# Optimization experiments

Measured on AMD Instinct MI355X. Metric: run time of the kernel, lower is better.

The kernel has to match this reference:

```python
import jax, jax.numpy as jnp
import numpy as np

B, N, E = 2, 5000, 160000
F_IN, HID, ED = 128, 128, 16
IN_EDGE = 2 * F_IN + 16 + ED  # source, target, radial(4*4), edge_attr


def _lin(k, fan_in, fan_out):
    return (jax.random.normal(k, (fan_in, fan_out), jnp.float32) / np.sqrt(fan_in)).astype(jnp.float32)


def setup_inputs() -> dict:
    key = jax.random.key(0)
    ks = jax.random.split(key, 16)
    h = jax.random.normal(ks[0], (B, N, F_IN), jnp.float32)
    coord = jax.random.normal(ks[1], (B, N, 4, 3), jnp.float32)
    edge_index = jax.random.randint(ks[2], (2, E), 0, N)
    edge_attr = jax.random.normal(ks[3], (E, ED), jnp.float32)
    return {
        "h": h, "coord": coord, "edge_index": edge_index, "edge_attr": edge_attr,
        # edge_mlp: Linear(IN_EDGE->HID), ReLU, Linear(HID->HID), ReLU
        "W_e1": _lin(ks[4], IN_EDGE, HID), "b_e1": jnp.zeros((HID,), jnp.float32),
        "W_e2": _lin(ks[5], HID, HID), "b_e2": jnp.zeros((HID,), jnp.float32),
        # node_mlp: Linear(HID+F_IN->HID), ReLU, Linear(HID->F_IN)
        "W_n1": _lin(ks[6], HID + F_IN, HID), "b_n1": jnp.zeros((HID,), jnp.float32),
        "W_n2": _lin(ks[7], HID, F_IN), "b_n2": jnp.zeros((F_IN,), jnp.float32),
        # coord_mlp: Linear(HID->HID), ReLU, Linear(HID->4, bias=False, xavier gain 0.001)
        "W_c1": _lin(ks[8], HID, HID), "b_c1": jnp.zeros((HID,), jnp.float32),
        "W_c2": _lin(ks[9], HID, 4) * 0.001,
    }


def reference(h, coord, edge_index, edge_attr,
              W_e1, b_e1, W_e2, b_e2,
              W_n1, b_n1, W_n2, b_n2,
              W_c1, b_c1, W_c2):
    row, col = edge_index[0], edge_index[1]
    coords_weight = 1.0
    n_nodes = h.shape[1]

    def single(h_b, coord_b):
        # coord2radial
        cd = coord_b[row] - coord_b[col]                                  # [E,4,3]
        prod = jnp.einsum('ejt,ekt->ejk', cd, cd).reshape(cd.shape[0], -1)  # [E,16]
        nrm = jnp.linalg.norm(prod, axis=-1, keepdims=True)
        radial = prod / jnp.maximum(nrm, 1e-12)                           # F.normalize
        # edge_model
        x = jnp.concatenate([h_b[row], h_b[col], radial, edge_attr], axis=-1)
        ef = jax.nn.relu(jax.nn.relu(x @ W_e1 + b_e1) @ W_e2 + b_e2)      # [E,HID]
        # coord_model: segment mean of cd * coord_mlp(ef)
        w = jax.nn.relu(ef @ W_c1 + b_c1) @ W_c2                          # [E,4]
        trans = cd * w[:, :, None]                                        # [E,4,3]
        agg_c = jax.ops.segment_sum(trans, row, num_segments=n_nodes)     # [N,4,3]
        cnt = jax.ops.segment_sum(jnp.ones((row.shape[0],), trans.dtype), row,
                                  num_segments=n_nodes)                   # [N]
        coord_new = coord_b + (agg_c / jnp.maximum(cnt, 1.0)[:, None, None]) * coords_weight
        # node_model (recurrent)
        agg_h = jax.ops.segment_sum(ef, row, num_segments=n_nodes)        # [N,HID]
        z = jnp.concatenate([h_b, agg_h], axis=-1)
        h_new = h_b + jax.nn.relu(z @ W_n1 + b_n1) @ W_n2 + b_n2
        return h_new, coord_new

    hs, coords = jax.vmap(single)(h, coord)
    return hs, coords
```

## Files before the change

### kernel.cpp

```cpp
#include <hip/hip_runtime.h>
#include <hip/hip_bf16.h>

#define B   2
#define NN_ 5000
#define NE_ 160000
#define F   128
#define HID 128
#define ED  16

typedef __bf16 bf16x8 __attribute__((ext_vector_type(8)));
typedef __bf16 bf16x4 __attribute__((ext_vector_type(4)));
typedef float  f32x4  __attribute__((ext_vector_type(4)));

#define MS  136
#define PS  40
#define EDG 64
#define ZS  264
#define HS  136
#define NPB2 32

__global__ __launch_bounds__(512) void pack_hist_kernel(
    const float* __restrict__ We1, const float* __restrict__ We2,
    const float* __restrict__ Wc1, const float* __restrict__ Wc2,
    const float* __restrict__ Wn1, const float* __restrict__ Wn2,
    const int* __restrict__ ei,
    const float* __restrict__ h, const float* __restrict__ be1,
    __bf16* __restrict__ pw1, __bf16* __restrict__ pw2,
    __bf16* __restrict__ pwc1, __bf16* __restrict__ pwc2,
    __bf16* __restrict__ pwn1, __bf16* __restrict__ pwn2,
    float4* __restrict__ agg4, int* __restrict__ csr_cnt,
    __bf16* __restrict__ pr, __bf16* __restrict__ pc)
{
    __shared__ __align__(16) __bf16 hs[128 * MS];
    const int t = threadIdx.x;

    if (blockIdx.x < 236) {
        int idx = blockIdx.x * 512 + t;
        const float* W; __bf16* P; int KT, Nr, local;
        if (idx < 36864)       { W = We1; P = pw1;  KT = 9; Nr = 128; local = idx; }
        else if (idx < 53248)  { W = We2; P = pw2;  KT = 4; Nr = 128; local = idx - 36864; }
        else if (idx < 69632)  { W = Wc1; P = pwc1; KT = 4; Nr = 128; local = idx - 53248; }
        else if (idx < 71680)  { W = Wc2; P = pwc2; KT = 4; Nr = 4;   local = idx - 69632; }
        else if (idx < 104448) { W = Wn1; P = pwn1; KT = 8; Nr = 128; local = idx - 71680; }
        else                   { W = Wn2; P = pwn2; KT = 4; Nr = 128; local = idx - 104448; }
        int j = local & 7, lane = (local >> 3) & 63, rest = local >> 9;
        int kt = rest % KT, nt = rest / KT;
        int k = kt * 32 + (lane >> 4) * 8 + j;
        int n = nt * 16 + (lane & 15);
        float v = (n < Nr) ? W[k * Nr + n] : 0.f;
        P[local] = (__bf16)v;
        float4 z4 = {0.f, 0.f, 0.f, 0.f};
        for (int i = idx; i < 350000; i += 120832) agg4[i] = z4;
        return;
    }
    if (blockIdx.x < 549) {
        int i = (blockIdx.x - 236) * 512 + t;
        if (i < NE_) atomicAdd(&csr_cnt[ei[i]], 1);
        return;
    }

    const int bp = blockIdx.x - 549;
    const int b = bp / 40;
    const int n0 = (bp % 40) * 128;
    const int lane = t & 63, wave = t >> 6;
    const int quad = lane >> 4, c = lane & 15;

    #pragma unroll
    for (int it = 0; it < 8; it++) {
        int idx = it * 512 + t;
        int node = idx >> 5, ch = idx & 31;
        int gn = n0 + node;
        float4 v = (gn < NN_) ? *(const float4*)&h[((size_t)b * NN_ + gn) * F + ch * 4]
                              : (float4){0.f, 0.f, 0.f, 0.f};
        bf16x4 bv = {(__bf16)v.x, (__bf16)v.y, (__bf16)v.z, (__bf16)v.w};
        *(bf16x4*)&hs[node * MS + ch * 4] = bv;
    }
    __syncthreads();

    f32x4 accr[8], accc[8];
    #pragma unroll
    for (int m = 0; m < 8; m++) { accr[m] = (f32x4){0,0,0,0}; accc[m] = (f32x4){0,0,0,0}; }
    for (int kt = 0; kt < 4; kt++) {
        bf16x8 wr, wc;
        #pragma unroll
        for (int jj = 0; jj < 8; jj++) {
            int k = kt * 32 + quad * 8 + jj;
            wr[jj] = (__bf16)We1[k * HID + wave * 16 + c];
            wc[jj] = (__bf16)We1[(k + 128) * HID + wave * 16 + c];
        }
        #pragma unroll
        for (int m = 0; m < 8; m++) {
            bf16x8 x = *(const bf16x8*)&hs[(m * 16 + c) * MS + kt * 32 + quad * 8];
            accr[m] = __builtin_amdgcn_mfma_f32_16x16x32_bf16(wr, x, accr[m], 0, 0, 0);
            accc[m] = __builtin_amdgcn_mfma_f32_16x16x32_bf16(wc, x, accc[m], 0, 0, 0);
        }
    }
    float4 bb = *(const float4*)&be1[wave * 16 + quad * 4];
    #pragma unroll
    for (int m = 0; m < 8; m++) {
        int gn = n0 + m * 16 + c;
        if (gn < NN_) {
            size_t base = ((size_t)b * NN_ + gn) * F + wave * 16 + quad * 4;
            bf16x4 orr = {(__bf16)(accr[m][0] + bb.x), (__bf16)(accr[m][1] + bb.y),
                          (__bf16)(accr[m][2] + bb.z), (__bf16)(accr[m][3] + bb.w)};
            bf16x4 occ = {(__bf16)accc[m][0], (__bf16)accc[m][1], (__bf16)accc[m][2], (__bf16)accc[m][3]};
            *(bf16x4*)&pr[base] = orr;
            *(bf16x4*)&pc[base] = occ;
        }
    }
}

__global__ __launch_bounds__(512) void scan_kernel(const int* __restrict__ csr_cnt,
                                                   int* __restrict__ csr_off, int* __restrict__ csr_pos)
{
    __shared__ int part[512];
    const int t = threadIdx.x;
    int sum = 0;
    #pragma unroll
    for (int j = 0; j < 10; j++) {
        int idx = t * 10 + j;
        if (idx < NN_) sum += csr_cnt[idx];
    }
    part[t] = sum;
    __syncthreads();
    for (int off = 1; off < 512; off <<= 1) {
        int v = (t >= off) ? part[t - off] : 0;
        __syncthreads();
        part[t] += v;
        __syncthreads();
    }
    int run = part[t] - sum;
    #pragma unroll
    for (int j = 0; j < 10; j++) {
        int idx = t * 10 + j;
        if (idx < NN_) { csr_off[idx] = run; csr_pos[idx] = run; run += csr_cnt[idx]; }
    }
    if (t == 0) csr_off[NN_] = NE_;
}

__global__ __launch_bounds__(512) void scatter_kernel(const int* __restrict__ ei,
                                                      int* __restrict__ csr_pos,
                                                      int* __restrict__ bucket)
{
    int i = blockIdx.x * 512 + threadIdx.x;
    if (i < NE_) {
        int p = atomicAdd(&csr_pos[ei[i]], 1);
        bucket[p] = i;
    }
}

__global__ __launch_bounds__(512, 6) void edge_kernel(
    const __bf16* __restrict__ pr, const __bf16* __restrict__ pc,
    const float* __restrict__ coord,
    const int* __restrict__ ei, const float* __restrict__ ea,
    const int* __restrict__ bucket,
    const float* __restrict__ be2, const float* __restrict__ bc1,
    const __bf16* __restrict__ pw1, const __bf16* __restrict__ pw2,
    const __bf16* __restrict__ pwc1, const __bf16* __restrict__ pwc2,
    float* __restrict__ agg_h, float* __restrict__ agg_c)
{
    __shared__ __align__(16) __bf16 buf1[EDG * MS];
    __shared__ __align__(16) __bf16 buf2[EDG * MS];
    __shared__ __bf16 cds[EDG][12];
    __shared__ int rs[EDG], cs[EDG], eids[EDG];

    const int t = threadIdx.x;
    const int b = blockIdx.y;
    const int p0 = blockIdx.x * EDG;
    const int lane = t & 63, wave = t >> 6;
    const int quad = lane >> 4, c = lane & 15;

    if (t < EDG) {
        int me = bucket[p0 + t];
        eids[t] = me;
        rs[t] = ei[me]; cs[t] = ei[NE_ + me];
    }
    __syncthreads();

    const __bf16* prb = pr + (size_t)b * NN_ * F;
    const __bf16* pcb = pc + (size_t)b * NN_ * F;
    #pragma unroll
    for (int it = 0; it < 2; it++) {
        int idx = it * 512 + t;
        int e = idx >> 4, ch = idx & 15;
        bf16x8 a = *(const bf16x8*)(prb + (size_t)rs[e] * F + ch * 8);
        bf16x8 v = *(const bf16x8*)(pcb + (size_t)cs[e] * F + ch * 8);
        bf16x8 o;
        #pragma unroll
        for (int j = 0; j < 8; j++) o[j] = (__bf16)((float)a[j] + (float)v[j]);
        *(bf16x8*)&buf1[e * MS + ch * 8] = o;
    }
    if (t < 256) {
        const int e4 = t >> 2, j4 = t & 3;
        const float* crp = coord + ((size_t)b * NN_ + rs[e4]) * 12 + j4 * 3;
        const float* ccp = coord + ((size_t)b * NN_ + cs[e4]) * 12 + j4 * 3;
        float cd0 = crp[0] - ccp[0], cd1 = crp[1] - ccp[1], cd2 = crp[2] - ccp[2];
        cds[e4][j4 * 3 + 0] = (__bf16)cd0;
        cds[e4][j4 * 3 + 1] = (__bf16)cd1;
        cds[e4][j4 * 3 + 2] = (__bf16)cd2;
        float px[4], ss = 0.f;
        #pragma unroll
        for (int k = 0; k < 4; k++) {
            int sl = (lane & ~3) | k;
            float bx = __shfl(cd0, sl, 64);
            float by = __shfl(cd1, sl, 64);
            float bz = __shfl(cd2, sl, 64);
            px[k] = cd0 * bx + cd1 * by + cd2 * bz;
            ss += px[k] * px[k];
        }
        ss += __shfl_xor(ss, 1, 64);
        ss += __shfl_xor(ss, 2, 64);
        float inv = 1.0f / fmaxf(sqrtf(ss), 1e-12f);
        bf16x4 xp = {(__bf16)(px[0] * inv), (__bf16)(px[1] * inv),
                     (__bf16)(px[2] * inv), (__bf16)(px[3] * inv)};
        *(bf16x4*)&buf2[e4 * PS + j4 * 4] = xp;
        float4 v = *(const float4*)(ea + (size_t)eids[e4] * ED + j4 * 4);
        bf16x4 bea = {(__bf16)v.x, (__bf16)v.y, (__bf16)v.z, (__bf16)v.w};
        *(bf16x4*)&buf2[e4 * PS + 16 + j4 * 4] = bea;
    }
    __syncthreads();

    const bf16x8* pw1v  = (const bf16x8*)pw1;
    const bf16x8* pw2v  = (const bf16x8*)pw2;
    const bf16x8* pwc1v = (const bf16x8*)pwc1;
    const bf16x8* pwc2v = (const bf16x8*)pwc2;

    f32x4 acc1[4];
    #pragma unroll
    for (int m = 0; m < 4; m++) acc1[m] = (f32x4){0,0,0,0};
    {
        bf16x8 w = pw1v[(wave * 9 + 8) * 64 + lane];
        #pragma unroll
        for (int m = 0; m < 4; m++) {
            bf16x8 x1 = *(const bf16x8*)&buf2[(m * 16 + c) * PS + quad * 8];
            acc1[m] = __builtin_amdgcn_mfma_f32_16x16x32_bf16(w, x1, acc1[m], 0, 0, 0);
        }
    }
    #pragma unroll
    for (int m = 0; m < 4; m++) {
        int row = m * 16 + c;
        bf16x4 pp = *(const bf16x4*)&buf1[row * MS + wave * 16 + quad * 4];
        bf16x4 o = { (__bf16)fmaxf(acc1[m][0] + (float)pp[0], 0.f),
                     (__bf16)fmaxf(acc1[m][1] + (float)pp[1], 0.f),
                     (__bf16)fmaxf(acc1[m][2] + (float)pp[2], 0.f),
                     (__bf16)fmaxf(acc1[m][3] + (float)pp[3], 0.f) };
        *(bf16x4*)&buf1[row * MS + wave * 16 + quad * 4] = o;
    }
    __syncthreads();

    f32x4 acc2[4];
    #pragma unroll
    for (int m = 0; m < 4; m++) acc2[m] = (f32x4){0,0,0,0};
    for (int kt = 0; kt < 4; kt++) {
        bf16x8 w = pw2v[(wave * 4 + kt) * 64 + lane];
        #pragma unroll
        for (int m = 0; m < 4; m++) {
            bf16x8 x = *(const bf16x8*)&buf1[(m * 16 + c) * MS + kt * 32 + quad * 8];
            acc2[m] = __builtin_amdgcn_mfma_f32_16x16x32_bf16(w, x, acc2[m], 0, 0, 0);
        }
    }
    {
        float4 bb = *(const float4*)&be2[wave * 16 + quad * 4];
        #pragma unroll
        for (int m = 0; m < 4; m++) {
            int row = m * 16 + c;
            bf16x4 o = { (__bf16)fmaxf(acc2[m][0] + bb.x, 0.f),
                         (__bf16)fmaxf(acc2[m][1] + bb.y, 0.f),
                         (__bf16)fmaxf(acc2[m][2] + bb.z, 0.f),
                         (__bf16)fmaxf(acc2[m][3] + bb.w, 0.f) };
            *(bf16x4*)&buf2[row * MS + wave * 16 + quad * 4] = o;
        }
    }
    __syncthreads();

    f32x4 acc3[4];
    #pragma unroll
    for (int m = 0; m < 4; m++) acc3[m] = (f32x4){0,0,0,0};
    for (int kt = 0; kt < 4; kt++) {
        bf16x8 w = pwc1v[(wave * 4 + kt) * 64 + lane];
        #pragma unroll
        for (int m = 0; m < 4; m++) {
            bf16x8 x = *(const bf16x8*)&buf2[(m * 16 + c) * MS + kt * 32 + quad * 8];
            acc3[m] = __builtin_amdgcn_mfma_f32_16x16x32_bf16(w, x, acc3[m], 0, 0, 0);
        }
    }
    {
        float4 bb = *(const float4*)&bc1[wave * 16 + quad * 4];
        #pragma unroll
        for (int m = 0; m < 4; m++) {
            int row = m * 16 + c;
            bf16x4 o = { (__bf16)fmaxf(acc3[m][0] + bb.x, 0.f),
                         (__bf16)fmaxf(acc3[m][1] + bb.y, 0.f),
                         (__bf16)fmaxf(acc3[m][2] + bb.z, 0.f),
                         (__bf16)fmaxf(acc3[m][3] + bb.w, 0.f) };
            *(bf16x4*)&buf1[row * MS + wave * 16 + quad * 4] = o;
        }
    }
    __syncthreads();

    if (wave < 4) {
        f32x4 accw = (f32x4){0,0,0,0};
        for (int kt = 0; kt < 4; kt++) {
            bf16x8 x = *(const bf16x8*)&buf1[(wave * 16 + c) * MS + kt * 32 + quad * 8];
            accw = __builtin_amdgcn_mfma_f32_16x16x32_bf16(pwc2v[kt * 64 + lane], x, accw, 0, 0, 0);
        }
        if (quad == 0) {
            int e = wave * 16 + c;
            #pragma unroll
            for (int j = 0; j < 12; j++)
                cds[e][j] = (__bf16)((float)cds[e][j] * accw[j / 3]);
        }
    }

    {
        float* aggh_b = agg_h + (size_t)b * NN_ * HID;
        const int col = t & 127, seg = t >> 7;
        float run = 0.f;
        int cur = rs[seg * 16];
        for (int e = seg * 16; e < seg * 16 + 16; e++) {
            int r = rs[e];
            float v = (float)buf2[e * MS + col];
            if (r != cur) {
                atomicAdd(&aggh_b[(size_t)cur * HID + col], run);
                run = 0.f; cur = r;
            }
            run += v;
        }
        atomicAdd(&aggh_b[(size_t)cur * HID + col], run);
    }
    __syncthreads();

    if (t < 24) {
        float* aggc_b = agg_c + (size_t)b * NN_ * 12;
        const int j = t % 12, q = t / 12;
        float run = 0.f;
        int cur = rs[q * 32];
        for (int e = q * 32; e < q * 32 + 32; e++) {
            int r = rs[e];
            float v = (float)cds[e][j];
            if (r != cur) {
                atomicAdd(&aggc_b[(size_t)cur * 12 + j], run);
                run = 0.f; cur = r;
            }
            run += v;
        }
        atomicAdd(&aggc_b[(size_t)cur * 12 + j], run);
    }
}

__global__ __launch_bounds__(256) void node_kernel(
    const float* __restrict__ h, const float* __restrict__ agg_h,
    const float* __restrict__ agg_c, const float* __restrict__ coord,
    const int* __restrict__ csr_off,
    const __bf16* __restrict__ pwn1, const float* __restrict__ bn1,
    const __bf16* __restrict__ pwn2, const float* __restrict__ bn2,
    float* __restrict__ out_h, float* __restrict__ out_c)
{
    __shared__ __align__(16) __bf16 zs[NPB2 * ZS];
    __shared__ __align__(16) __bf16 h1s[NPB2 * HS];
    const int t = threadIdx.x;
    const int b = blockIdx.y;
    const int n0 = blockIdx.x * NPB2;
    const int lane = t & 63, wave = t >> 6;
    const int quad = lane >> 4, c = lane & 15;

    #pragma unroll
    for (int it = 0; it < 8; it++) {
        int idx = it * 256 + t;
        int node = idx >> 6, ch = idx & 63;
        int gn = n0 + node;
        float4 v = (float4){0.f, 0.f, 0.f, 0.f};
        if (gn < NN_) {
            const float* src = (ch < 32) ? &h[((size_t)b * NN_ + gn) * F + ch * 4]
                                         : &agg_h[((size_t)b * NN_ + gn) * HID + (ch - 32) * 4];
            v = *(const float4*)src;
        }
        bf16x4 bv = {(__bf16)v.x, (__bf16)v.y, (__bf16)v.z, (__bf16)v.w};
        *(bf16x4*)&zs[node * ZS + ch * 4] = bv;
    }
    __syncthreads();

    const bf16x8* w1v = (const bf16x8*)pwn1;
    const bf16x8* w2v = (const bf16x8*)pwn2;
    f32x4 a1[2][2];
    #pragma unroll
    for (int m = 0; m < 2; m++)
        #pragma unroll
        for (int n = 0; n < 2; n++) a1[m][n] = (f32x4){0,0,0,0};
    for (int kt = 0; kt < 8; kt++) {
        bf16x8 x[2];
        #pragma unroll
        for (int m = 0; m < 2; m++)
            x[m] = *(const bf16x8*)&zs[(m * 16 + c) * ZS + kt * 32 + quad * 8];
        #pragma unroll
        for (int n = 0; n < 2; n++) {
            bf16x8 w = w1v[((2 * wave + n) * 8 + kt) * 64 + lane];
            #pragma unroll
            for (int m = 0; m < 2; m++)
                a1[m][n] = __builtin_amdgcn_mfma_f32_16x16x32_bf16(w, x[m], a1[m][n], 0, 0, 0);
        }
    }
    __syncthreads();
    #pragma unroll
    for (int n = 0; n < 2; n++) {
        int nt = 2 * wave + n;
        float4 bb = *(const float4*)&bn1[nt * 16 + quad * 4];
        #pragma unroll
        for (int m = 0; m < 2; m++) {
            bf16x4 o = { (__bf16)fmaxf(a1[m][n][0] + bb.x, 0.f),
                         (__bf16)fmaxf(a1[m][n][1] + bb.y, 0.f),
                         (__bf16)fmaxf(a1[m][n][2] + bb.z, 0.f),
                         (__bf16)fmaxf(a1[m][n][3] + bb.w, 0.f) };
            *(bf16x4*)&h1s[(m * 16 + c) * HS + nt * 16 + quad * 4] = o;
        }
    }
    __syncthreads();

    f32x4 a2[2][2];
    #pragma unroll
    for (int m = 0; m < 2; m++)
        #pragma unroll
        for (int n = 0; n < 2; n++) a2[m][n] = (f32x4){0,0,0,0};
    for (int kt = 0; kt < 4; kt++) {
        bf16x8 x[2];
        #pragma unroll
        for (int m = 0; m < 2; m++)
            x[m] = *(const bf16x8*)&h1s[(m * 16 + c) * HS + kt * 32 + quad * 8];
        #pragma unroll
        for (int n = 0; n < 2; n++) {
            bf16x8 w = w2v[((2 * wave + n) * 4 + kt) * 64 + lane];
            #pragma unroll
            for (int m = 0; m < 2; m++)
                a2[m][n] = __builtin_amdgcn_mfma_f32_16x16x32_bf16(w, x[m], a2[m][n], 0, 0, 0);
        }
    }
    float* os = (float*)zs;
    #pragma unroll
    for (int n = 0; n < 2; n++) {
        int nt = 2 * wave + n;
        float4 bb = *(const float4*)&bn2[nt * 16 + quad * 4];
        #pragma unroll
        for (int m = 0; m < 2; m++) {
            f32x4 o = { a2[m][n][0] + bb.x, a2[m][n][1] + bb.y,
                        a2[m][n][2] + bb.z, a2[m][n][3] + bb.w };
            *(f32x4*)&os[(m * 16 + c) * 132 + nt * 16 + quad * 4] = o;
        }
    }
    __syncthreads();

    #pragma unroll
    for (int it = 0; it < 4; it++) {
        int idx = it * 256 + t;
        int node = idx >> 5, ch = idx & 31;
        int gn = n0 + node;
        if (gn < NN_) {
            size_t gb = ((size_t)b * NN_ + gn) * F + ch * 4;
            float4 hres = *(const float4*)&h[gb];
            float4 acc = *(const float4*)&os[node * 132 + ch * 4];
            float4 o = { hres.x + acc.x, hres.y + acc.y, hres.z + acc.z, hres.w + acc.w };
            *(float4*)&out_h[gb] = o;
        }
    }
    for (int idx = t; idx < NPB2 * 12; idx += 256) {
        int node = idx / 12, j = idx % 12;
        int gn = n0 + node;
        if (gn < NN_) {
            float deg = (float)(csr_off[gn + 1] - csr_off[gn]);
            size_t ci = ((size_t)b * NN_ + gn) * 12 + j;
            out_c[ci] = coord[ci] + agg_c[ci] / fmaxf(deg, 1.0f);
        }
    }
}

extern "C" void kernel_launch(void* const* d_in, const int* in_sizes, int n_in,
                              void* d_out, int out_size, void* d_ws, size_t ws_size,
                              hipStream_t stream) {
    const float* h     = (const float*)d_in[0];
    const float* coord = (const float*)d_in[1];
    const int*   ei    = (const int*)d_in[2];
    const float* ea    = (const float*)d_in[3];
    const float* We1   = (const float*)d_in[4];
    const float* be1   = (const float*)d_in[5];
    const float* We2   = (const float*)d_in[6];
    const float* be2   = (const float*)d_in[7];
    const float* Wn1   = (const float*)d_in[8];
    const float* bn1   = (const float*)d_in[9];
    const float* Wn2   = (const float*)d_in[10];
    const float* bn2   = (const float*)d_in[11];
    const float* Wc1   = (const float*)d_in[12];
    const float* bc1   = (const float*)d_in[13];
    const float* Wc2   = (const float*)d_in[14];

    float* out_h = (float*)d_out;
    float* out_c = out_h + (size_t)B * NN_ * F;

    unsigned char* base = (unsigned char*)d_ws;
    __bf16* pw1  = (__bf16*)base;
    __bf16* pw2  = pw1 + 36864;
    __bf16* pwc1 = pw2 + 16384;
    __bf16* pwc2 = pwc1 + 16384;
    __bf16* pwn1 = pwc2 + 2048;
    __bf16* pwn2 = pwn1 + 32768;
    unsigned char* dyn = base + 241664;

    int* csr_cnt = (int*)(dyn);
    int* csr_off = (int*)(dyn + 20000);
    int* csr_pos = (int*)(dyn + 40016);
    int* bucket  = (int*)(dyn + 60016);
    float* agg_h = (float*)(dyn + 700016);
    float* agg_c = agg_h + (size_t)B * NN_ * HID;
    __bf16* pr   = (__bf16*)(agg_c + (size_t)B * NN_ * 12);
    __bf16* pc   = pr + (size_t)B * NN_ * F;

    hipMemsetAsync(csr_cnt, 0, 20000, stream);

    pack_hist_kernel<<<629, 512, 0, stream>>>(We1, We2, Wc1, Wc2, Wn1, Wn2, ei, h, be1,
                                              pw1, pw2, pwc1, pwc2, pwn1, pwn2,
                                              (float4*)agg_h, csr_cnt, pr, pc);

    scan_kernel<<<1, 512, 0, stream>>>(csr_cnt, csr_off, csr_pos);

    scatter_kernel<<<313, 512, 0, stream>>>(ei, csr_pos, bucket);

    dim3 eg(NE_ / EDG, B);
    edge_kernel<<<eg, 512, 0, stream>>>(pr, pc, coord, ei, ea, bucket, be2, bc1,
                                        pw1, pw2, pwc1, pwc2, agg_h, agg_c);

    dim3 ng((NN_ + NPB2 - 1) / NPB2, B);
    node_kernel<<<ng, 256, 0, stream>>>(h, agg_h, agg_c, coord, csr_off,
                                        pwn1, bn1, pwn2, bn2, out_h, out_c);
}
```

Before: 197.8 us.

## Fuse scan and scatter via grid barrier; overlap agg_h reduction with coord MLP

Merges the single-block prefix scan and the edge scatter into one kernel. Block 0 computes the CSR offsets, then all blocks wait on a two-level global barrier built from atomics before scattering, which saves one kernel launch and its gap. Separately, in the edge kernel the agg_h segmented reduction now runs on waves 4-7 while waves 0-3 compute the coord MLP, rather than after it. The barrier relies on all 313 blocks being co-resident and uses relaxed atomics without explicit fences, which risks deadlock or ordering problems.

```diff
diff --git a/kernel.cpp b/kernel.cpp
--- a/kernel.cpp
+++ b/kernel.cpp
@@ -18,6 +18,8 @@
 #define ZS  264
 #define HS  136
 #define NPB2 32
+#define NB_B 313
+#define NGRP_B 10
 
 __global__ __launch_bounds__(512) void pack_hist_kernel(
     const float* __restrict__ We1, const float* __restrict__ We2,
@@ -110,39 +112,69 @@
     }
 }
 
-__global__ __launch_bounds__(512) void scan_kernel(const int* __restrict__ csr_cnt,
-                                                   int* __restrict__ csr_off, int* __restrict__ csr_pos)
+__global__ __launch_bounds__(512) void scan_scatter_kernel(
+    const int* __restrict__ csr_cnt, int* csr_off, int* csr_pos,
+    const int* __restrict__ ei, int* __restrict__ bucket, int* bar)
 {
-    __shared__ int part[512];
     const int t = threadIdx.x;
-    int sum = 0;
-    #pragma unroll
-    for (int j = 0; j < 10; j++) {
-        int idx = t * 10 + j;
-        if (idx < NN_) sum += csr_cnt[idx];
-    }
-    part[t] = sum;
-    __syncthreads();
-    for (int off = 1; off < 512; off <<= 1) {
-        int v = (t >= off) ? part[t - off] : 0;
+    const int blk = blockIdx.x;
+
+    if (blk == 0) {
+        __shared__ int part[512];
+        int sum = 0;
+        #pragma unroll
+        for (int j = 0; j < 10; j++) {
+            int idx = t * 10 + j;
+            if (idx < NN_) sum += csr_cnt[idx];
+        }
+        part[t] = sum;
         __syncthreads();
-        part[t] += v;
-        __syncthreads();
-    }
-    int run = part[t] - sum;
-    #pragma unroll
-    for (int j = 0; j < 10; j++) {
-        int idx = t * 10 + j;
-        if (idx < NN_) { csr_off[idx] = run; csr_pos[idx] = run; run += csr_cnt[idx]; }
-    }
-    if (t == 0) csr_off[NN_] = NE_;
-}
-
-__global__ __launch_bounds__(512) void scatter_kernel(const int* __restrict__ ei,
-                                                      int* __restrict__ csr_pos,
-                                                      int* __restrict__ bucket)
-{
-    int i = blockIdx.x * 512 + threadIdx.x;
+        for (int off = 1; off < 512; off <<= 1) {
+            int v = (t >= off) ? part[t - off] : 0;
+            __syncthreads();
+            part[t] += v;
+            __syncthreads();
+        }
+        int run = part[t] - sum;
+        #pragma unroll
+        for (int j = 0; j < 10; j++) {
+            int idx = t * 10 + j;
+            if (idx < NN_) {
+                atomicExch(&csr_off[idx], run);
+                atomicExch(&csr_pos[idx], run);
+                run += csr_cnt[idx];
+            }
+        }
+        if (t == 0) atomicExch(&csr_off[NN_], NE_);
+    }
+
+    __syncthreads();
+    if (t == 0) {
+        const int g = blk >> 5;
+        const int gsz = (g == NGRP_B - 1) ? (NB_B - g * 32) : 32;
+        int* rootcnt = bar;
+        int* rootgen = bar + 64;
+        int* gcnt    = bar + 128 + g * 64;
+        int* ggen    = bar + 128 + NGRP_B * 64 + g * 64;
+        int a = __hip_atomic_fetch_add(gcnt, 1, __ATOMIC_RELAXED, __HIP_MEMORY_SCOPE_AGENT);
+        if (a == gsz - 1) {
+            int r = __hip_atomic_fetch_add(rootcnt, 1, __ATOMIC_RELAXED, __HIP_MEMORY_SCOPE_AGENT);
+            if (r == NGRP_B - 1) {
+                __hip_atomic_fetch_add(rootgen, 1, __ATOMIC_RELAXED, __HIP_MEMORY_SCOPE_AGENT);
+            } else {
+                while (__hip_atomic_fetch_add(rootgen, 0, __ATOMIC_RELAXED, __HIP_MEMORY_SCOPE_AGENT) < 1)
+                    __builtin_amdgcn_s_sleep(8);
+            }
+            __hip_atomic_fetch_add(ggen, 1, __ATOMIC_RELAXED, __HIP_MEMORY_SCOPE_AGENT);
+        } else {
+            while (__hip_atomic_fetch_add(ggen, 0, __ATOMIC_RELAXED, __HIP_MEMORY_SCOPE_AGENT) < 1)
+                __builtin_amdgcn_s_sleep(8);
+        }
+    }
+    asm volatile("" ::: "memory");
+    __syncthreads();
+
+    int i = blk * 512 + t;
     if (i < NE_) {
         int p = atomicAdd(&csr_pos[ei[i]], 1);
         bucket[p] = i;
@@ -310,14 +342,12 @@
             for (int j = 0; j < 12; j++)
                 cds[e][j] = (__bf16)((float)cds[e][j] * accw[j / 3]);
         }
-    }
-
-    {
+    } else {
         float* aggh_b = agg_h + (size_t)b * NN_ * HID;
-        const int col = t & 127, seg = t >> 7;
+        const int col = t & 127, seg = (t >> 7) - 2;
         float run = 0.f;
-        int cur = rs[seg * 16];
-        for (int e = seg * 16; e < seg * 16 + 16; e++) {
+        int cur = rs[seg * 32];
+        for (int e = seg * 32; e < seg * 32 + 32; e++) {
             int r = rs[e];
             float v = (float)buf2[e * MS + col];
             if (r != cur) {
@@ -504,23 +534,22 @@
     unsigned char* dyn = base + 241664;
 
     int* csr_cnt = (int*)(dyn);
-    int* csr_off = (int*)(dyn + 20000);
-    int* csr_pos = (int*)(dyn + 40016);
-    int* bucket  = (int*)(dyn + 60016);
-    float* agg_h = (float*)(dyn + 700016);
+    int* bar     = (int*)(dyn + 20000);
+    int* csr_off = (int*)(dyn + 28192);
+    int* csr_pos = (int*)(dyn + 48208);
+    int* bucket  = (int*)(dyn + 68208);
+    float* agg_h = (float*)(dyn + 708208);
     float* agg_c = agg_h + (size_t)B * NN_ * HID;
     __bf16* pr   = (__bf16*)(agg_c + (size_t)B * NN_ * 12);
     __bf16* pc   = pr + (size_t)B * NN_ * F;
 
-    hipMemsetAsync(csr_cnt, 0, 20000, stream);
+    hipMemsetAsync(dyn, 0, 28192, stream);
 
     pack_hist_kernel<<<629, 512, 0, stream>>>(We1, We2, Wc1, Wc2, Wn1, Wn2, ei, h, be1,
                                               pw1, pw2, pwc1, pwc2, pwn1, pwn2,
                                               (float4*)agg_h, csr_cnt, pr, pc);
 
-    scan_kernel<<<1, 512, 0, stream>>>(csr_cnt, csr_off, csr_pos);
-
-    scatter_kernel<<<313, 512, 0, stream>>>(ei, csr_pos, bucket);
+    scan_scatter_kernel<<<NB_B, 512, 0, stream>>>(csr_cnt, csr_off, csr_pos, ei, bucket, bar);
 
     dim3 eg(NE_ / EDG, B);
     edge_kernel<<<eg, 512, 0, stream>>>(pr, pc, coord, ei, ea, bucket, be2, bc1,
```

Result: no change. 200.8 us (+1.5%).
